# Kernel tuning notes

Hardware: AMD Instinct MI355X
Metric: run time of the kernel (lower is better)

## Reference

```python
import jax, jax.numpy as jnp
import numpy as np

NUM_PT = 13
NUM_SQ = 64
SQPT = NUM_SQ * NUM_PT            # 832
NUM_FEATURES = NUM_SQ * SQPT      # 53248
ATTN_TABLE = NUM_SQ * SQPT * SQPT # 44302336
DEPTH = 256
DFF = 1024
NUM_HEADS = 4
N = 512
LN_EPS = 1e-5


def layer_norm(x, w, b):
    m = jnp.mean(x, axis=-1, keepdims=True)
    v = jnp.mean(jnp.square(x - m), axis=-1, keepdims=True)
    return (x - m) * jax.lax.rsqrt(v + LN_EPS) * w + b


def setup_inputs() -> dict:
    key = jax.random.key(0)
    ks = jax.random.split(key, 12)
    # indices must satisfy piece_indices = ksq*832 + offset, offset in [0,832)
    pno = jax.random.randint(ks[0], (N, NUM_SQ), 0, SQPT, dtype=jnp.int32)
    ksq = jax.random.randint(ks[1], (N,), 0, NUM_SQ, dtype=jnp.int32)
    piece_indices = ksq[:, None] * SQPT + pno
    attn_bias_indices = jax.random.randint(ks[2], (N, NUM_SQ * NUM_SQ), 0, NUM_PT * NUM_PT, dtype=jnp.int32)
    f32 = jnp.float32
    return {
        "piece_indices": piece_indices,
        "attn_bias_indices": attn_bias_indices,
        "ksq": ksq,
        "value_table": jax.random.normal(ks[3], (NUM_FEATURES, DEPTH), f32) * 0.02,
        "attn_weights_table": jax.random.normal(ks[4], (ATTN_TABLE, NUM_HEADS), f32) * 0.02,
        "attn_bias_table": jax.random.normal(ks[5], (NUM_PT * NUM_PT, NUM_HEADS), f32) * 0.02,
        "attn_scale": jnp.asarray(100.0, f32),
        "W1": jax.random.normal(ks[6], (DEPTH, DFF), f32) * 0.02,
        "b1": jnp.zeros((DFF,), f32),
        "W2": jax.random.normal(ks[7], (DFF, DEPTH), f32) * 0.02,
        "b2": jnp.zeros((DEPTH,), f32),
        "ln1_w": jnp.ones((DEPTH,), f32),
        "ln1_b": jnp.zeros((DEPTH,), f32),
        "ln2_w": jnp.ones((DEPTH,), f32),
        "ln2_b": jnp.zeros((DEPTH,), f32),
    }


def reference(piece_indices, attn_bias_indices, ksq, value_table, attn_weights_table,
              attn_bias_table, attn_scale, W1, b1, W2, b2, ln1_w, ln1_b, ln2_w, ln2_b):
    n = piece_indices.shape[0]
    dh = DEPTH // NUM_HEADS
    pno = piece_indices - ksq[:, None] * SQPT                      # [N,64] in [0,832)
    attn_idx = (pno[:, :, None] * SQPT + pno[:, None, :]
                + ksq[:, None, None] * SQPT * SQPT)                # [N,64,64]
    aw = attn_weights_table[attn_idx]                              # [N,64,64,H]
    abi = attn_bias_indices.reshape(n, NUM_SQ, NUM_SQ).transpose(0, 2, 1)
    ab = attn_bias_table[abi]                                      # [N,64,64,H]
    logits = ((aw + ab) * attn_scale).transpose(0, 3, 1, 2)        # [N,H,64,64]
    attn = jax.nn.softmax(logits, axis=-1)
    values = value_table[piece_indices].reshape(n, NUM_SQ, NUM_HEADS, dh).transpose(0, 2, 1, 3)  # [N,H,64,dh]
    ctx = jnp.einsum('nhqk,nhkd->nhqd', attn, values) + values
    x = layer_norm(ctx.transpose(0, 2, 1, 3).reshape(n, NUM_SQ, DEPTH), ln1_w, ln1_b)
    ffn = jnp.maximum(x @ W1 + b1, 0.0) @ W2 + b2
    return layer_norm(ffn + x, ln2_w, ln2_b)
```

## Files before the change

### kernel.cpp

```cpp
#include <hip/hip_runtime.h>
#include <stdint.h>

typedef unsigned short u16;
typedef __attribute__((ext_vector_type(8))) short bf16x8;
typedef __attribute__((ext_vector_type(4))) float f32x4;

typedef __attribute__((address_space(1))) const unsigned char gas_u8;
typedef __attribute__((address_space(3))) unsigned char las_u8;

__device__ __forceinline__ void gload_lds16(const void* g, void* l) {
  __builtin_amdgcn_global_load_lds((const gas_u8*)g, (las_u8*)l, 16, 0, 0);
}

__device__ __forceinline__ u16 f2bf(float f) {
  uint32_t u = __float_as_uint(f);
  u += 0x7fffu + ((u >> 16) & 1u);
  return (u16)(u >> 16);
}
__device__ __forceinline__ float bf2f(u16 v) {
  return __uint_as_float(((uint32_t)v) << 16);
}

__global__ __launch_bounds__(256, 4)
void transpose_kernel(const float* __restrict__ W1, u16* __restrict__ W1T,
                      const float* __restrict__ W2, u16* __restrict__ W2T) {
  __shared__ u16 tile[64 * 66];
  int b = blockIdx.x;
  const float* src; u16* dst; int R, C, tc, tr;
  if (b < 64) { src = W1; dst = W1T; R = 256; C = 1024; tc = (b & 15) * 64; tr = (b >> 4) * 64; }
  else { b -= 64; src = W2; dst = W2T; R = 1024; C = 256; tc = (b & 3) * 64; tr = (b >> 2) * 64; }
  const int t = threadIdx.x;
  const int c = t & 63, rb = t >> 6;
#pragma unroll
  for (int i = 0; i < 16; ++i) {
    int r = i * 4 + rb;
    tile[r * 66 + c] = f2bf(src[(size_t)(tr + r) * C + tc + c]);
  }
  __syncthreads();
#pragma unroll
  for (int i = 0; i < 16; ++i) {
    int x = i * 4 + rb;
    int y = c;
    dst[(size_t)(tc + x) * R + tr + y] = tile[y * 66 + x];
  }
}

__global__ __launch_bounds__(256, 2)
void attn_kernel(const int* __restrict__ piece_indices,
                 const int* __restrict__ abi_idx,
                 const int* __restrict__ ksq,
                 const float* __restrict__ value_table,
                 const float* __restrict__ aw_table,
                 const float* __restrict__ ab_table,
                 const float* __restrict__ scale_p,
                 const float* __restrict__ ln1w, const float* __restrict__ ln1b,
                 u16* __restrict__ xout) {
  __shared__ __align__(16) u16 VT[256 * 64];
  __shared__ __align__(16) u16 P[4 * 64 * 64];
  __shared__ __align__(16) float abt_s[169 * 4];
  __shared__ int pno_s[64];
  __shared__ int pidx_s[64];
  __shared__ float red[4][64][2];
  __shared__ float redA[4][4][64];
  __shared__ float redB[4][4][64];

  const int n = blockIdx.x;
  const int t = threadIdx.x;
  const int h = t >> 6;
  const int lane = t & 63;
  const int ks = ksq[n];

  if (t < 64) {
    int pi = piece_indices[n * 64 + t];
    pidx_s[t] = pi;
    pno_s[t] = pi - ks * 832;
  }
  for (int i = t; i < 676; i += 256) abt_s[i] = ab_table[i];
  __syncthreads();

  const float scale = scale_p[0];
  const int q = lane, kg = h;

  float l[4][16];
  {
    const int base = ks * (832 * 832) + pno_s[q] * 832;
#pragma unroll
    for (int j = 0; j < 16; ++j) {
      int k = kg * 16 + j;
      int idx = base + pno_s[k];
      f32x4 aw4 = *(const f32x4*)(aw_table + (size_t)idx * 4);
      int bi = abi_idx[n * 4096 + k * 64 + q];
      f32x4 ab4 = *(const f32x4*)(abt_s + bi * 4);
#pragma unroll
      for (int hh = 0; hh < 4; ++hh) l[hh][j] = (aw4[hh] + ab4[hh]) * scale;
    }
  }

  {
    const int feat = t;
#pragma unroll
    for (int c = 0; c < 8; ++c) {
      bf16x8 vv;
#pragma unroll
      for (int j = 0; j < 8; ++j) {
        int k = c * 8 + j;
        float v = value_table[(size_t)pidx_s[k] * 256 + feat];
        vv[j] = (short)f2bf(v);
      }
      int off = feat * 64 + ((c ^ (feat & 7)) << 3);
      *(bf16x8*)(&VT[off]) = vv;
    }
  }

#pragma unroll
  for (int hh = 0; hh < 4; ++hh) {
    float m = l[hh][0];
#pragma unroll
    for (int j = 1; j < 16; ++j) m = fmaxf(m, l[hh][j]);
    redA[kg][hh][q] = m;
  }
  __syncthreads();
  float inv[4];
#pragma unroll
  for (int hh = 0; hh < 4; ++hh) {
    float m = fmaxf(fmaxf(redA[0][hh][q], redA[1][hh][q]),
                    fmaxf(redA[2][hh][q], redA[3][hh][q]));
    float s = 0.f;
#pragma unroll
    for (int j = 0; j < 16; ++j) { l[hh][j] = __expf(l[hh][j] - m); s += l[hh][j]; }
    redB[kg][hh][q] = s;
  }
  __syncthreads();
#pragma unroll
  for (int hh = 0; hh < 4; ++hh)
    inv[hh] = 1.f / (redB[0][hh][q] + redB[1][hh][q] + redB[2][hh][q] + redB[3][hh][q]);

#pragma unroll
  for (int hh = 0; hh < 4; ++hh) {
#pragma unroll
    for (int c2 = 0; c2 < 2; ++c2) {
      int c = kg * 2 + c2;
      bf16x8 pv;
#pragma unroll
      for (int j8 = 0; j8 < 8; ++j8) {
        int j = c2 * 8 + j8;
        int k = kg * 16 + j;
        float v = l[hh][j] * inv[hh] + ((k == q) ? 1.f : 0.f);
        pv[j8] = (short)f2bf(v);
      }
      int off = (hh * 64 + q) * 64 + ((c ^ (q & 7)) << 3);
      *(bf16x8*)(&P[off]) = pv;
    }
  }
  __syncthreads();

  const int li = lane & 15, lg = lane >> 4;
  f32x4 acc[4][4] = {};
#pragma unroll
  for (int kst = 0; kst < 2; ++kst) {
    int cg = kst * 4 + lg;
    bf16x8 aF[4], bF[4];
#pragma unroll
    for (int mi = 0; mi < 4; ++mi) {
      int row = mi * 16 + li;
      aF[mi] = *(const bf16x8*)(&P[(h * 64 + row) * 64 + ((cg ^ (row & 7)) << 3)]);
    }
#pragma unroll
    for (int ni = 0; ni < 4; ++ni) {
      int rr = h * 64 + ni * 16 + li;
      bF[ni] = *(const bf16x8*)(&VT[rr * 64 + ((cg ^ (rr & 7)) << 3)]);
    }
#pragma unroll
    for (int mi = 0; mi < 4; ++mi)
#pragma unroll
      for (int ni = 0; ni < 4; ++ni)
        acc[mi][ni] = __builtin_amdgcn_mfma_f32_16x16x32_bf16(aF[mi], bF[ni], acc[mi][ni], 0, 0, 0);
  }

#pragma unroll
  for (int mi = 0; mi < 4; ++mi)
#pragma unroll
    for (int r = 0; r < 4; ++r) {
      float s1 = 0.f, s2 = 0.f;
#pragma unroll
      for (int ni = 0; ni < 4; ++ni) { float v = acc[mi][ni][r]; s1 += v; s2 += v * v; }
#pragma unroll
      for (int mk = 1; mk < 16; mk <<= 1) { s1 += __shfl_xor(s1, mk, 64); s2 += __shfl_xor(s2, mk, 64); }
      if (li == 0) { int q2 = mi * 16 + lg * 4 + r; red[h][q2][0] = s1; red[h][q2][1] = s2; }
    }
  __syncthreads();

  float w_[4], b_[4];
#pragma unroll
  for (int ni = 0; ni < 4; ++ni) {
    int f = h * 64 + ni * 16 + li;
    w_[ni] = ln1w[f]; b_[ni] = ln1b[f];
  }
#pragma unroll
  for (int mi = 0; mi < 4; ++mi)
#pragma unroll
    for (int r = 0; r < 4; ++r) {
      int q2 = mi * 16 + lg * 4 + r;
      float S1 = red[0][q2][0] + red[1][q2][0] + red[2][q2][0] + red[3][q2][0];
      float S2 = red[0][q2][1] + red[1][q2][1] + red[2][q2][1] + red[3][q2][1];
      float mean = S1 * (1.f / 256.f);
      float var = S2 * (1.f / 256.f) - mean * mean;
      float rs = rsqrtf(var + 1e-5f);
      size_t tb = (size_t)(n * 64 + q2) * 256;
#pragma unroll
      for (int ni = 0; ni < 4; ++ni) {
        float xv = (acc[mi][ni][r] - mean) * rs * w_[ni] + b_[ni];
        xout[tb + h * 64 + ni * 16 + li] = f2bf(xv);
      }
    }
}

__global__ __launch_bounds__(256, 2)
void ffn_fused_kernel(const u16* __restrict__ X, const u16* __restrict__ W1T,
                      const u16* __restrict__ W2T,
                      const float* __restrict__ b1, const float* __restrict__ b2,
                      const float* __restrict__ ln2w, const float* __restrict__ ln2b,
                      float* __restrict__ out) {
  __shared__ __align__(16) u16 Xl[64 * 256];
  __shared__ __align__(16) u16 Wb[64 * 256];
  __shared__ __align__(16) u16 Hb[64 * 64];
  __shared__ float red[4][64][2];

  const int t = threadIdx.x;
  const int wv = t >> 6, lane = t & 63;
  const int li = lane & 15, lg = lane >> 4;
  const int m0 = blockIdx.x * 64;
  f32x4 oacc[4][4] = {};

#pragma unroll
  for (int it = 0; it < 8; ++it) {
    int idx = it * 256 + t;
    int row = idx >> 5, c = idx & 31;
    const u16* g = X + (size_t)(m0 + row) * 256 + (((c ^ (row & 7)) & 31) << 3);
    gload_lds16(g, (char*)Xl + it * 4096 + wv * 1024);
  }

  for (int ch = 0; ch < 16; ++ch) {
#pragma unroll
    for (int it = 0; it < 8; ++it) {
      int idx = it * 256 + t;
      int row = idx >> 5, c = idx & 31;
      const u16* g = W1T + (size_t)(ch * 64 + row) * 256 + (((c ^ (row & 7)) & 31) << 3);
      gload_lds16(g, (char*)Wb + it * 4096 + wv * 1024);
    }
    __syncthreads();

    f32x4 hacc[4] = {};
#pragma unroll
    for (int kst = 0; kst < 8; ++kst) {
      int cg = kst * 4 + lg;
      bf16x8 aF[4], bF;
      {
        int brow = wv * 16 + li;
        bF = *(const bf16x8*)((char*)Wb + brow * 512 + (((cg ^ (brow & 7)) & 31) << 4));
      }
#pragma unroll
      for (int mi = 0; mi < 4; ++mi) {
        int row = mi * 16 + li;
        aF[mi] = *(const bf16x8*)((char*)Xl + row * 512 + (((cg ^ (row & 7)) & 31) << 4));
      }
#pragma unroll
      for (int mi = 0; mi < 4; ++mi)
        hacc[mi] = __builtin_amdgcn_mfma_f32_16x16x32_bf16(aF[mi], bF, hacc[mi], 0, 0, 0);
    }
    __syncthreads();

    {
      float bv = b1[ch * 64 + wv * 16 + li];
      int col = wv * 16 + li;
      int c2 = col >> 3;
#pragma unroll
      for (int mi = 0; mi < 4; ++mi)
#pragma unroll
        for (int r = 0; r < 4; ++r) {
          int row = mi * 16 + lg * 4 + r;
          float v = fmaxf(hacc[mi][r] + bv, 0.f);
          *(u16*)((char*)Hb + row * 128 + ((c2 ^ (row & 7)) << 4) + (col & 7) * 2) = f2bf(v);
        }
    }
#pragma unroll
    for (int it = 0; it < 8; ++it) {
      int idx = it * 256 + t;
      int row = idx >> 3, c = idx & 7;
      const u16* g = W2T + (size_t)row * 1024 + ch * 64 + ((c ^ (row & 7)) << 3);
      gload_lds16(g, (char*)Wb + it * 4096 + wv * 1024);
    }
    __syncthreads();

#pragma unroll
    for (int kst = 0; kst < 2; ++kst) {
      int cg = kst * 4 + lg;
      bf16x8 aF[4], bF[4];
#pragma unroll
      for (int mi = 0; mi < 4; ++mi) {
        int row = mi * 16 + li;
        aF[mi] = *(const bf16x8*)((char*)Hb + row * 128 + (((cg ^ (row & 7)) & 7) << 4));
      }
#pragma unroll
      for (int ni = 0; ni < 4; ++ni) {
        int row = wv * 64 + ni * 16 + li;
        bF[ni] = *(const bf16x8*)((char*)Wb + row * 128 + (((cg ^ (row & 7)) & 7) << 4));
      }
#pragma unroll
      for (int mi = 0; mi < 4; ++mi)
#pragma unroll
        for (int ni = 0; ni < 4; ++ni)
          oacc[mi][ni] = __builtin_amdgcn_mfma_f32_16x16x32_bf16(aF[mi], bF[ni], oacc[mi][ni], 0, 0, 0);
    }
    __syncthreads();
  }

  float bias2[4];
#pragma unroll
  for (int ni = 0; ni < 4; ++ni) bias2[ni] = b2[wv * 64 + ni * 16 + li];

#pragma unroll
  for (int mi = 0; mi < 4; ++mi)
#pragma unroll
    for (int r = 0; r < 4; ++r) {
      float s1 = 0.f, s2 = 0.f;
      int row = mi * 16 + lg * 4 + r;
#pragma unroll
      for (int ni = 0; ni < 4; ++ni) {
        int col = wv * 64 + ni * 16 + li;
        int cc = col >> 3;
        u16 xres = *(const u16*)((char*)Xl + row * 512 + (((cc ^ (row & 7)) & 31) << 4) + (col & 7) * 2);
        float v = oacc[mi][ni][r] + bias2[ni] + bf2f(xres);
        oacc[mi][ni][r] = v;
        s1 += v; s2 += v * v;
      }
#pragma unroll
      for (int mk = 1; mk < 16; mk <<= 1) { s1 += __shfl_xor(s1, mk, 64); s2 += __shfl_xor(s2, mk, 64); }
      if (li == 0) { int q2 = mi * 16 + lg * 4 + r; red[wv][q2][0] = s1; red[wv][q2][1] = s2; }
    }
  __syncthreads();

  float lw[4], lb[4];
#pragma unroll
  for (int ni = 0; ni < 4; ++ni) {
    int col = wv * 64 + ni * 16 + li;
    lw[ni] = ln2w[col]; lb[ni] = ln2b[col];
  }
#pragma unroll
  for (int mi = 0; mi < 4; ++mi)
#pragma unroll
    for (int r = 0; r < 4; ++r) {
      int q2 = mi * 16 + lg * 4 + r;
      float S1 = red[0][q2][0] + red[1][q2][0] + red[2][q2][0] + red[3][q2][0];
      float S2 = red[0][q2][1] + red[1][q2][1] + red[2][q2][1] + red[3][q2][1];
      float mean = S1 * (1.f / 256.f);
      float var = S2 * (1.f / 256.f) - mean * mean;
      float rs = rsqrtf(var + 1e-5f);
      size_t rbase = (size_t)(m0 + q2) * 256;
#pragma unroll
      for (int ni = 0; ni < 4; ++ni)
        out[rbase + wv * 64 + ni * 16 + li] = (oacc[mi][ni][r] - mean) * rs * lw[ni] + lb[ni];
    }
}

extern "C" void kernel_launch(void* const* d_in, const int* in_sizes, int n_in,
                              void* d_out, int out_size, void* d_ws, size_t ws_size,
                              hipStream_t stream) {
  const int* piece_indices = (const int*)d_in[0];
  const int* abi_idx       = (const int*)d_in[1];
  const int* ksq           = (const int*)d_in[2];
  const float* value_table = (const float*)d_in[3];
  const float* aw_table    = (const float*)d_in[4];
  const float* ab_table    = (const float*)d_in[5];
  const float* attn_scale  = (const float*)d_in[6];
  const float* W1          = (const float*)d_in[7];
  const float* b1          = (const float*)d_in[8];
  const float* W2          = (const float*)d_in[9];
  const float* b2          = (const float*)d_in[10];
  const float* ln1w        = (const float*)d_in[11];
  const float* ln1b        = (const float*)d_in[12];
  const float* ln2w        = (const float*)d_in[13];
  const float* ln2b        = (const float*)d_in[14];

  char* ws = (char*)d_ws;
  u16* W1T = (u16*)(ws);
  u16* W2T = (u16*)(ws + (512 << 10));
  u16* X   = (u16*)(ws + (1 << 20));
  float* out = (float*)d_out;

  transpose_kernel<<<128, 256, 0, stream>>>(W1, W1T, W2, W2T);
  attn_kernel<<<512, 256, 0, stream>>>(piece_indices, abi_idx, ksq, value_table,
                                       aw_table, ab_table, attn_scale, ln1w, ln1b, X);
  ffn_fused_kernel<<<512, 256, 0, stream>>>(X, W1T, W2T, b1, b2, ln2w, ln2b, out);
}
```

Measured before the change: 119.0 us.

## Fuse attention and FFN kernels into one kernel sharing LDS

Merges the attention+LN1 kernel and the fused FFN+LN2 kernel into a single kernel per 64-row block. The LN1 output is written as bf16 straight into a swizzled LDS tile that the FFN stage reads, which removes the global X round trip and one launch. A single manually laid-out LDS buffer is reused across the two stages (about 78 KB). The risk is lower occupancy and a longer kernel with more register pressure, and attention and FFN phases can no longer overlap across kernels.

```diff
diff --git a/kernel.cpp b/kernel.cpp
--- a/kernel.cpp
+++ b/kernel.cpp
@@ -45,8 +45,17 @@
   }
 }
 
+#define SM_BASE 65536
+#define OFF_ABT  (SM_BASE + 0)
+#define OFF_PNO  (SM_BASE + 2704)
+#define OFF_PIDX (SM_BASE + 2960)
+#define OFF_REDA (SM_BASE + 3216)
+#define OFF_REDB (SM_BASE + 7312)
+#define OFF_RED  (SM_BASE + 11408)
+#define OFF_HB   (SM_BASE + 0)
+
 __global__ __launch_bounds__(256, 2)
-void attn_kernel(const int* __restrict__ piece_indices,
+void mega_kernel(const int* __restrict__ piece_indices,
                  const int* __restrict__ abi_idx,
                  const int* __restrict__ ksq,
                  const float* __restrict__ value_table,
@@ -54,15 +63,19 @@
                  const float* __restrict__ ab_table,
                  const float* __restrict__ scale_p,
                  const float* __restrict__ ln1w, const float* __restrict__ ln1b,
-                 u16* __restrict__ xout) {
-  __shared__ __align__(16) u16 VT[256 * 64];
-  __shared__ __align__(16) u16 P[4 * 64 * 64];
-  __shared__ __align__(16) float abt_s[169 * 4];
-  __shared__ int pno_s[64];
-  __shared__ int pidx_s[64];
-  __shared__ float red[4][64][2];
-  __shared__ float redA[4][4][64];
-  __shared__ float redB[4][4][64];
+                 const u16* __restrict__ W1T, const u16* __restrict__ W2T,
+                 const float* __restrict__ b1, const float* __restrict__ b2,
+                 const float* __restrict__ ln2w, const float* __restrict__ ln2b,
+                 float* __restrict__ out) {
+  __shared__ __align__(16) char SMEM[79872];
+  u16* VT = (u16*)(SMEM);
+  u16* P  = (u16*)(SMEM + 32768);
+  float* abt_s = (float*)(SMEM + OFF_ABT);
+  int* pno_s   = (int*)(SMEM + OFF_PNO);
+  int* pidx_s  = (int*)(SMEM + OFF_PIDX);
+  float* redA  = (float*)(SMEM + OFF_REDA);
+  float* redB  = (float*)(SMEM + OFF_REDB);
+  float* red   = (float*)(SMEM + OFF_RED);
 
   const int n = blockIdx.x;
   const int t = threadIdx.x;
@@ -117,23 +130,24 @@
     float m = l[hh][0];
 #pragma unroll
     for (int j = 1; j < 16; ++j) m = fmaxf(m, l[hh][j]);
-    redA[kg][hh][q] = m;
+    redA[(kg * 4 + hh) * 64 + q] = m;
   }
   __syncthreads();
   float inv[4];
 #pragma unroll
   for (int hh = 0; hh < 4; ++hh) {
-    float m = fmaxf(fmaxf(redA[0][hh][q], redA[1][hh][q]),
-                    fmaxf(redA[2][hh][q], redA[3][hh][q]));
+    float m = fmaxf(fmaxf(redA[(0 * 4 + hh) * 64 + q], redA[(1 * 4 + hh) * 64 + q]),
+                    fmaxf(redA[(2 * 4 + hh) * 64 + q], redA[(3 * 4 + hh) * 64 + q]));
     float s = 0.f;
 #pragma unroll
     for (int j = 0; j < 16; ++j) { l[hh][j] = __expf(l[hh][j] - m); s += l[hh][j]; }
-    redB[kg][hh][q] = s;
+    redB[(kg * 4 + hh) * 64 + q] = s;
   }
   __syncthreads();
 #pragma unroll
   for (int hh = 0; hh < 4; ++hh)
-    inv[hh] = 1.f / (redB[0][hh][q] + redB[1][hh][q] + redB[2][hh][q] + redB[3][hh][q]);
+    inv[hh] = 1.f / (redB[(0 * 4 + hh) * 64 + q] + redB[(1 * 4 + hh) * 64 + q] +
+                     redB[(2 * 4 + hh) * 64 + q] + redB[(3 * 4 + hh) * 64 + q]);
 
 #pragma unroll
   for (int hh = 0; hh < 4; ++hh) {
@@ -186,59 +200,44 @@
       for (int ni = 0; ni < 4; ++ni) { float v = acc[mi][ni][r]; s1 += v; s2 += v * v; }
 #pragma unroll
       for (int mk = 1; mk < 16; mk <<= 1) { s1 += __shfl_xor(s1, mk, 64); s2 += __shfl_xor(s2, mk, 64); }
-      if (li == 0) { int q2 = mi * 16 + lg * 4 + r; red[h][q2][0] = s1; red[h][q2][1] = s2; }
-    }
-  __syncthreads();
-
-  float w_[4], b_[4];
-#pragma unroll
-  for (int ni = 0; ni < 4; ++ni) {
-    int f = h * 64 + ni * 16 + li;
-    w_[ni] = ln1w[f]; b_[ni] = ln1b[f];
-  }
-#pragma unroll
-  for (int mi = 0; mi < 4; ++mi)
-#pragma unroll
-    for (int r = 0; r < 4; ++r) {
-      int q2 = mi * 16 + lg * 4 + r;
-      float S1 = red[0][q2][0] + red[1][q2][0] + red[2][q2][0] + red[3][q2][0];
-      float S2 = red[0][q2][1] + red[1][q2][1] + red[2][q2][1] + red[3][q2][1];
-      float mean = S1 * (1.f / 256.f);
-      float var = S2 * (1.f / 256.f) - mean * mean;
-      float rs = rsqrtf(var + 1e-5f);
-      size_t tb = (size_t)(n * 64 + q2) * 256;
-#pragma unroll
-      for (int ni = 0; ni < 4; ++ni) {
-        float xv = (acc[mi][ni][r] - mean) * rs * w_[ni] + b_[ni];
-        xout[tb + h * 64 + ni * 16 + li] = f2bf(xv);
-      }
-    }
-}
-
-__global__ __launch_bounds__(256, 2)
-void ffn_fused_kernel(const u16* __restrict__ X, const u16* __restrict__ W1T,
-                      const u16* __restrict__ W2T,
-                      const float* __restrict__ b1, const float* __restrict__ b2,
-                      const float* __restrict__ ln2w, const float* __restrict__ ln2b,
-                      float* __restrict__ out) {
-  __shared__ __align__(16) u16 Xl[64 * 256];
-  __shared__ __align__(16) u16 Wb[64 * 256];
-  __shared__ __align__(16) u16 Hb[64 * 64];
-  __shared__ float red[4][64][2];
-
-  const int t = threadIdx.x;
-  const int wv = t >> 6, lane = t & 63;
-  const int li = lane & 15, lg = lane >> 4;
-  const int m0 = blockIdx.x * 64;
+      if (li == 0) { int q2 = mi * 16 + lg * 4 + r; red[(h * 64 + q2) * 2 + 0] = s1; red[(h * 64 + q2) * 2 + 1] = s2; }
+    }
+  __syncthreads();
+
+  u16* Xl = (u16*)(SMEM + 32768);
+  {
+    float w_[4], b_[4];
+#pragma unroll
+    for (int ni = 0; ni < 4; ++ni) {
+      int f = h * 64 + ni * 16 + li;
+      w_[ni] = ln1w[f]; b_[ni] = ln1b[f];
+    }
+#pragma unroll
+    for (int mi = 0; mi < 4; ++mi)
+#pragma unroll
+      for (int r = 0; r < 4; ++r) {
+        int q2 = mi * 16 + lg * 4 + r;
+        float S1 = red[(0 * 64 + q2) * 2] + red[(1 * 64 + q2) * 2] +
+                   red[(2 * 64 + q2) * 2] + red[(3 * 64 + q2) * 2];
+        float S2 = red[(0 * 64 + q2) * 2 + 1] + red[(1 * 64 + q2) * 2 + 1] +
+                   red[(2 * 64 + q2) * 2 + 1] + red[(3 * 64 + q2) * 2 + 1];
+        float mean = S1 * (1.f / 256.f);
+        float var = S2 * (1.f / 256.f) - mean * mean;
+        float rs = rsqrtf(var + 1e-5f);
+#pragma unroll
+        for (int ni = 0; ni < 4; ++ni) {
+          int col = h * 64 + ni * 16 + li;
+          float xv = (acc[mi][ni][r] - mean) * rs * w_[ni] + b_[ni];
+          int cc = col >> 3;
+          *(u16*)((char*)Xl + q2 * 512 + (((cc ^ (q2 & 7)) & 31) << 4) + (col & 7) * 2) = f2bf(xv);
+        }
+      }
+  }
+
+  u16* Wb = (u16*)(SMEM);
+  u16* Hb = (u16*)(SMEM + OFF_HB);
+  const int wv = h;
   f32x4 oacc[4][4] = {};
-
-#pragma unroll
-  for (int it = 0; it < 8; ++it) {
-    int idx = it * 256 + t;
-    int row = idx >> 5, c = idx & 31;
-    const u16* g = X + (size_t)(m0 + row) * 256 + (((c ^ (row & 7)) & 31) << 3);
-    gload_lds16(g, (char*)Xl + it * 4096 + wv * 1024);
-  }
 
   for (int ch = 0; ch < 16; ++ch) {
 #pragma unroll
@@ -336,7 +335,7 @@
       }
 #pragma unroll
       for (int mk = 1; mk < 16; mk <<= 1) { s1 += __shfl_xor(s1, mk, 64); s2 += __shfl_xor(s2, mk, 64); }
-      if (li == 0) { int q2 = mi * 16 + lg * 4 + r; red[wv][q2][0] = s1; red[wv][q2][1] = s2; }
+      if (li == 0) { int q2 = mi * 16 + lg * 4 + r; red[(wv * 64 + q2) * 2 + 0] = s1; red[(wv * 64 + q2) * 2 + 1] = s2; }
     }
   __syncthreads();
 
@@ -351,12 +350,14 @@
 #pragma unroll
     for (int r = 0; r < 4; ++r) {
       int q2 = mi * 16 + lg * 4 + r;
-      float S1 = red[0][q2][0] + red[1][q2][0] + red[2][q2][0] + red[3][q2][0];
-      float S2 = red[0][q2][1] + red[1][q2][1] + red[2][q2][1] + red[3][q2][1];
+      float S1 = red[(0 * 64 + q2) * 2] + red[(1 * 64 + q2) * 2] +
+                 red[(2 * 64 + q2) * 2] + red[(3 * 64 + q2) * 2];
+      float S2 = red[(0 * 64 + q2) * 2 + 1] + red[(1 * 64 + q2) * 2 + 1] +
+                 red[(2 * 64 + q2) * 2 + 1] + red[(3 * 64 + q2) * 2 + 1];
       float mean = S1 * (1.f / 256.f);
       float var = S2 * (1.f / 256.f) - mean * mean;
       float rs = rsqrtf(var + 1e-5f);
-      size_t rbase = (size_t)(m0 + q2) * 256;
+      size_t rbase = (size_t)(n * 64 + q2) * 256;
 #pragma unroll
       for (int ni = 0; ni < 4; ++ni)
         out[rbase + wv * 64 + ni * 16 + li] = (oacc[mi][ni][r] - mean) * rs * lw[ni] + lb[ni];
@@ -385,11 +386,10 @@
   char* ws = (char*)d_ws;
   u16* W1T = (u16*)(ws);
   u16* W2T = (u16*)(ws + (512 << 10));
-  u16* X   = (u16*)(ws + (1 << 20));
   float* out = (float*)d_out;
 
   transpose_kernel<<<128, 256, 0, stream>>>(W1, W1T, W2, W2T);
-  attn_kernel<<<512, 256, 0, stream>>>(piece_indices, abi_idx, ksq, value_table,
-                                       aw_table, ab_table, attn_scale, ln1w, ln1b, X);
-  ffn_fused_kernel<<<512, 256, 0, stream>>>(X, W1T, W2T, b1, b2, ln2w, ln2b, out);
-}
+  mega_kernel<<<512, 256, 0, stream>>>(piece_indices, abi_idx, ksq, value_table,
+                                       aw_table, ab_table, attn_scale, ln1w, ln1b,
+                                       W1T, W2T, b1, b2, ln2w, ln2b, out);
+}
```

New measurement: 115.2 us. -3.3%, faster.
